# Performance work log

Measured on AMD Instinct MI355X. Metric: run time of the kernel, lower is better.

Reference implementation:

```python
import jax, jax.numpy as jnp
import numpy as np

BETA_VQ = 0.25
NUM_CODES = 1024
CODE_DIM = 256

def setup_inputs() -> dict:
    key = jax.random.key(0)
    k1, k2 = jax.random.split(key)
    z_e = jax.random.normal(k1, (64, 32, 32, CODE_DIM), dtype=jnp.float32)
    codebook = jax.random.uniform(k2, (NUM_CODES, CODE_DIM), dtype=jnp.float32,
                                  minval=-1.0 / NUM_CODES, maxval=1.0 / NUM_CODES)
    return {"z_e": z_e, "codebook": codebook}


def reference(z_e, codebook):
    B, H, W, D = z_e.shape
    z_flat = z_e.reshape(-1, D)  # [N, D], N = B*H*W
    # squared-euclidean distances via expansion: ||z||^2 + ||c||^2 - 2 z.c
    dist = (jnp.sum(z_flat ** 2, axis=1, keepdims=True)
            + jnp.sum(codebook ** 2, axis=1)
            - 2.0 * z_flat @ codebook.T)  # [N, num_codes]
    indices = jnp.argmin(dist, axis=1)  # [N]
    z_q = codebook[indices].reshape(z_e.shape)  # [B,H,W,D]
    codebook_loss = jnp.mean((jax.lax.stop_gradient(z_e) - z_q) ** 2)
    commit_loss = BETA_VQ * jnp.mean((z_e - jax.lax.stop_gradient(z_q)) ** 2)
    vq_loss = codebook_loss + commit_loss
    z_q_st = z_e + jax.lax.stop_gradient(z_q - z_e)  # straight-through
    indices = indices.reshape(B, H, W)
    return (z_q_st, vq_loss, indices)
```

## Files before the change

kernel.cpp:

```cpp
#include <hip/hip_runtime.h>
#include <hip/hip_bf16.h>


constexpr int D     = 256;
constexpr int NC    = 1024;
constexpr int NROWS = 65536;
constexpr int RPB   = 32;
constexpr int NBLK  = NROWS / RPB;
constexpr int ZS    = 264;
constexpr int QCAP  = 512;
#define MARGIN_Q 3.8e-3f

typedef float accv4  __attribute__((ext_vector_type(4)));
typedef short short8 __attribute__((ext_vector_type(8)));

__device__ __forceinline__ short f2bf(float x) {
    __hip_bfloat16 h = __float2bfloat16(x);
    return *reinterpret_cast<short*>(&h);
}
__device__ __forceinline__ unsigned packtrunc(float x, float y) {
    return (__float_as_uint(x) >> 16) | (__float_as_uint(y) & 0xffff0000u);
}

__device__ __forceinline__ float np_pairwise_sq128(const float* __restrict__ x) {
    float r[8];
    #pragma unroll
    for (int j = 0; j < 8; ++j) r[j] = __fmul_rn(x[j], x[j]);
    #pragma unroll
    for (int i = 8; i < 128; i += 8)
        #pragma unroll
        for (int j = 0; j < 8; ++j)
            r[j] = __fadd_rn(r[j], __fmul_rn(x[i + j], x[i + j]));
    float s01 = __fadd_rn(r[0], r[1]);
    float s23 = __fadd_rn(r[2], r[3]);
    float s45 = __fadd_rn(r[4], r[5]);
    float s67 = __fadd_rn(r[6], r[7]);
    return __fadd_rn(__fadd_rn(s01, s23), __fadd_rn(s45, s67));
}

__global__ void c2_kernel(const float* __restrict__ cb, float* __restrict__ c2) {
    int t = blockIdx.x * blockDim.x + threadIdx.x;
    if (t < NC) {
        const float* x = cb + (size_t)t * D;
        c2[t] = __fadd_rn(np_pairwise_sq128(x), np_pairwise_sq128(x + 128));
    }
}

__global__ void swz_kernel(const float* __restrict__ cb, short* __restrict__ swz) {
    int t = blockIdx.x * blockDim.x + threadIdx.x;
    int lane = t & 63, ts = t >> 6;
    int ks = ts & 7, tile = ts >> 3;
    int code = tile * 16 + (lane & 15);
    int kb   = ks * 32 + (lane >> 4) * 8;
    const float* src = cb + (size_t)code * D + kb;
    union { short s[8]; short8 v; } u;
    #pragma unroll
    for (int j = 0; j < 8; ++j) u.s[j] = f2bf(src[j]);
    *((short8*)swz + t) = u.v;
}

__global__ __launch_bounds__(256, 2) void vq_kernel(
    const float* __restrict__ z,
    const float* __restrict__ cb,
    const short* __restrict__ cb_swz,
    const float* __restrict__ c2g,
    float*       __restrict__ out_zq,
    float*       __restrict__ out_idx,
    double*      __restrict__ partials)
{
    __shared__ __align__(16) float z_lds[RPB][ZS];
    __shared__ float a_row[RPB];
    __shared__ __align__(16) float scratchA[RPB][4];
    __shared__ float c2_lds[NC];
    __shared__ int   rm_shared[RPB];
    __shared__ __align__(16) int queue[QCAP];
    __shared__ int   qn;

    const int tid     = threadIdx.x;
    const int lane    = tid & 63;
    const int w       = tid >> 6;
    const int rowBase = blockIdx.x * RPB;

    #pragma unroll
    for (int j = 0; j < 8; ++j) {
        int l = tid + 256 * j;
        int row = l >> 6, q = l & 63;
        float4 v = *(const float4*)(z + (size_t)(rowBase + row) * D + q * 4);
        *(float4*)&z_lds[row][q * 4] = v;
    }
    #pragma unroll
    for (int j = 0; j < 4; ++j) c2_lds[tid + 256 * j] = c2g[tid + 256 * j];
    if (tid < RPB) rm_shared[tid] = 0x7f800000;
    if (tid == 0)  qn = 0;
    __syncthreads();

    if (tid < RPB * 4) {
        int row = tid >> 2, q = tid & 3;
        int h = (q >> 1) * 128, p = (q & 1) * 4;
        const float* x = &z_lds[row][0];
        float r0 = __fmul_rn(x[h+p+0], x[h+p+0]);
        float r1 = __fmul_rn(x[h+p+1], x[h+p+1]);
        float r2 = __fmul_rn(x[h+p+2], x[h+p+2]);
        float r3 = __fmul_rn(x[h+p+3], x[h+p+3]);
        #pragma unroll
        for (int i = 8; i < 128; i += 8) {
            r0 = __fadd_rn(r0, __fmul_rn(x[h+i+p+0], x[h+i+p+0]));
            r1 = __fadd_rn(r1, __fmul_rn(x[h+i+p+1], x[h+i+p+1]));
            r2 = __fadd_rn(r2, __fmul_rn(x[h+i+p+2], x[h+i+p+2]));
            r3 = __fadd_rn(r3, __fmul_rn(x[h+i+p+3], x[h+i+p+3]));
        }
        scratchA[row][q] = __fadd_rn(__fadd_rn(r0, r1), __fadd_rn(r2, r3));
    }
    __syncthreads();
    if (tid < RPB) {
        float half0 = __fadd_rn(scratchA[tid][0], scratchA[tid][1]);
        float half1 = __fadd_rn(scratchA[tid][2], scratchA[tid][3]);
        a_row[tid]  = __fadd_rn(half0, half1);
    }
    __syncthreads();

    short8 afrag[2][8];
    #pragma unroll
    for (int rt = 0; rt < 2; ++rt)
        #pragma unroll
        for (int ks = 0; ks < 8; ++ks) {
            const float* src = z + (size_t)(rowBase + rt * 16 + (lane & 15)) * D
                                 + ks * 32 + (lane >> 4) * 8;
            float4 v0 = *(const float4*)(src);
            float4 v1 = *(const float4*)(src + 4);
            union { unsigned u[4]; short8 v; } pk;
            pk.u[0] = packtrunc(v0.x, v0.y);
            pk.u[1] = packtrunc(v0.z, v0.w);
            pk.u[2] = packtrunc(v1.x, v1.y);
            pk.u[3] = packtrunc(v1.z, v1.w);
            afrag[rt][ks] = pk.v;
        }
    float a_reg[2][4];
    #pragma unroll
    for (int rt = 0; rt < 2; ++rt)
        #pragma unroll
        for (int i = 0; i < 4; ++i)
            a_reg[rt][i] = a_row[rt * 16 + (lane >> 4) * 4 + i];

    float runmin[2][4];
    #pragma unroll
    for (int rt = 0; rt < 2; ++rt)
        #pragma unroll
        for (int i = 0; i < 4; ++i) runmin[rt][i] = 3.4e38f;

    unsigned kpk[16][2][2];
    const short8* bbase = (const short8*)cb_swz + lane;
    short8 bcur[8];
    #pragma unroll
    for (int ks = 0; ks < 8; ++ks) bcur[ks] = bbase[(size_t)w * 512 + ks * 64];

    #pragma unroll
    for (int t = 0; t < 16; ++t) {
        const int tile = w + 4 * t;
        short8 bnxt[8];
        if (t < 15) {
            #pragma unroll
            for (int ks = 0; ks < 8; ++ks)
                bnxt[ks] = bbase[(size_t)(tile + 4) * 512 + ks * 64];
        }
        accv4 acc[2];
        #pragma unroll
        for (int rt = 0; rt < 2; ++rt) acc[rt] = (accv4){0.f, 0.f, 0.f, 0.f};
        #pragma unroll
        for (int ks = 0; ks < 8; ++ks) {
            #pragma unroll
            for (int rt = 0; rt < 2; ++rt)
                acc[rt] = __builtin_amdgcn_mfma_f32_16x16x32_bf16(
                    afrag[rt][ks], bcur[ks], acc[rt], 0, 0, 0);
        }
        const float c2v = c2_lds[tile * 16 + (lane & 15)];
        #pragma unroll
        for (int rt = 0; rt < 2; ++rt) {
            float m0 = fmaf(2.0f, acc[rt][0], -c2v);
            float m1 = fmaf(2.0f, acc[rt][1], -c2v);
            float m2 = fmaf(2.0f, acc[rt][2], -c2v);
            float m3 = fmaf(2.0f, acc[rt][3], -c2v);
            kpk[t][rt][0] = packtrunc(m0, m1);
            kpk[t][rt][1] = packtrunc(m2, m3);
            runmin[rt][0] = fminf(runmin[rt][0], a_reg[rt][0] - m0);
            runmin[rt][1] = fminf(runmin[rt][1], a_reg[rt][1] - m1);
            runmin[rt][2] = fminf(runmin[rt][2], a_reg[rt][2] - m2);
            runmin[rt][3] = fminf(runmin[rt][3], a_reg[rt][3] - m3);
        }
        if (t < 15) {
            #pragma unroll
            for (int ks = 0; ks < 8; ++ks) bcur[ks] = bnxt[ks];
        }
    }

    #pragma unroll
    for (int rt = 0; rt < 2; ++rt)
        #pragma unroll
        for (int i = 0; i < 4; ++i) {
            float m = runmin[rt][i];
            m = fminf(m, __shfl_xor(m, 1));
            m = fminf(m, __shfl_xor(m, 2));
            m = fminf(m, __shfl_xor(m, 4));
            m = fminf(m, __shfl_xor(m, 8));
            if ((lane & 15) == 0) {
                int row = rt * 16 + (lane >> 4) * 4 + i;
                atomicMin(&rm_shared[row], __float_as_int(m));
            }
        }
    __syncthreads();

    float mthr[2][4];
    #pragma unroll
    for (int rt = 0; rt < 2; ++rt)
        #pragma unroll
        for (int i = 0; i < 4; ++i) {
            int row = rt * 16 + (lane >> 4) * 4 + i;
            mthr[rt][i] = a_reg[rt][i]
                        - (__int_as_float(rm_shared[row]) + MARGIN_Q);
        }
    #pragma unroll
    for (int t = 0; t < 16; ++t) {
        const int code = (w + 4 * t) * 16 + (lane & 15);
        #pragma unroll
        for (int rt = 0; rt < 2; ++rt)
            #pragma unroll
            for (int pr = 0; pr < 2; ++pr) {
                unsigned pk = kpk[t][rt][pr];
                float mlo = __uint_as_float(pk << 16);
                float mhi = __uint_as_float(pk & 0xffff0000u);
                if (mlo >= mthr[rt][2 * pr]) {
                    int row  = rt * 16 + (lane >> 4) * 4 + 2 * pr;
                    int slot = atomicAdd(&qn, 1);
                    if (slot < QCAP) queue[slot] = (row << 10) | code;
                }
                if (mhi >= mthr[rt][2 * pr + 1]) {
                    int row  = rt * 16 + (lane >> 4) * 4 + 2 * pr + 1;
                    int slot = atomicAdd(&qn, 1);
                    if (slot < QCAP) queue[slot] = (row << 10) | code;
                }
            }
    }

    unsigned long long* best64 = (unsigned long long*)&scratchA[0][0];
    if (tid < RPB) best64[tid] = ~0ull;
    __syncthreads();
    int total = qn;
    if (total <= QCAP) {
        for (int t = tid; t < total; t += 256) {
            int e = queue[t];
            int row = e >> 10, code = e & 1023;
            const float4* cp = (const float4*)(cb + (size_t)code * D);
            const float*  zr = &z_lds[row][0];
            float acc = 0.0f;
            #pragma unroll 8
            for (int d4 = 0; d4 < 64; ++d4) {
                float4 cv = cp[d4];
                acc = fmaf(zr[d4 * 4 + 0], cv.x, acc);
                acc = fmaf(zr[d4 * 4 + 1], cv.y, acc);
                acc = fmaf(zr[d4 * 4 + 2], cv.z, acc);
                acc = fmaf(zr[d4 * 4 + 3], cv.w, acc);
            }
            float key = __fsub_rn(__fadd_rn(a_row[row], c2_lds[code]), 2.0f * acc);
            unsigned long long pk =
                ((unsigned long long)__float_as_uint(key) << 32) | (unsigned)code;
            atomicMin(&best64[row], pk);
        }
    } else {
        for (int r = 0; r < RPB; ++r) {
            for (int c = tid; c < NC; c += 256) {
                const float4* cp = (const float4*)(cb + (size_t)c * D);
                const float*  zr = &z_lds[r][0];
                float acc = 0.0f;
                #pragma unroll 8
                for (int d4 = 0; d4 < 64; ++d4) {
                    float4 cv = cp[d4];
                    acc = fmaf(zr[d4 * 4 + 0], cv.x, acc);
                    acc = fmaf(zr[d4 * 4 + 1], cv.y, acc);
                    acc = fmaf(zr[d4 * 4 + 2], cv.z, acc);
                    acc = fmaf(zr[d4 * 4 + 3], cv.w, acc);
                }
                float key = __fsub_rn(__fadd_rn(a_row[r], c2_lds[c]), 2.0f * acc);
                unsigned long long pk =
                    ((unsigned long long)__float_as_uint(key) << 32) | (unsigned)c;
                atomicMin(&best64[r], pk);
            }
        }
    }
    __syncthreads();

    int* winner = rm_shared;
    if (tid < RPB) {
        unsigned long long b = best64[tid];
        int wdx = (b == ~0ull) ? 0 : (int)(b & 0xffffffffu);
        winner[tid] = wdx;
        out_idx[rowBase + tid] = (float)wdx;
    }
    __syncthreads();

    double lacc = 0.0;
    #pragma unroll
    for (int j = 0; j < 8; ++j) {
        int idx = tid + 256 * j;
        int row = idx >> 6;
        int q4  = idx & 63;
        int wd  = winner[row];
        float4 cv = *(const float4*)(cb + (size_t)wd * D + q4 * 4);
        float4 zv = *(const float4*)&z_lds[row][q4 * 4];
        float4 o;
        o.x = __fadd_rn(zv.x, __fsub_rn(cv.x, zv.x));
        o.y = __fadd_rn(zv.y, __fsub_rn(cv.y, zv.y));
        o.z = __fadd_rn(zv.z, __fsub_rn(cv.z, zv.z));
        o.w = __fadd_rn(zv.w, __fsub_rn(cv.w, zv.w));
        *(float4*)(out_zq + (size_t)(rowBase + row) * D + q4 * 4) = o;
        double d0 = (double)zv.x - (double)cv.x;
        double d1 = (double)zv.y - (double)cv.y;
        double d2 = (double)zv.z - (double)cv.z;
        double d3 = (double)zv.w - (double)cv.w;
        lacc += d0 * d0 + d1 * d1 + d2 * d2 + d3 * d3;
    }
    __syncthreads();
    double* dred = (double*)&queue[0];
    dred[tid] = lacc;
    __syncthreads();
    for (int s = 128; s > 0; s >>= 1) {
        if (tid < s) dred[tid] += dred[tid + s];
        __syncthreads();
    }
    if (tid == 0) partials[blockIdx.x] = dred[0];
}

__global__ void loss_kernel(const double* __restrict__ partials,
                            float* __restrict__ out_loss)
{
    __shared__ double sm[256];
    int tid = threadIdx.x;
    double s = 0.0;
    for (int i = tid; i < NBLK; i += 256) s += partials[i];
    sm[tid] = s;
    __syncthreads();
    for (int k = 128; k > 0; k >>= 1) {
        if (tid < k) sm[tid] += sm[tid + k];
        __syncthreads();
    }
    if (tid == 0)
        out_loss[0] = (float)(1.25 * sm[0] / (double)((size_t)NROWS * D));
}

extern "C" void kernel_launch(void* const* d_in, const int* in_sizes, int n_in,
                              void* d_out, int out_size, void* d_ws, size_t ws_size,
                              hipStream_t stream)
{
    const float* z  = (const float*)d_in[0];
    const float* cb = (const float*)d_in[1];

    float* out      = (float*)d_out;
    float* out_zq   = out;
    float* out_loss = out + (size_t)NROWS * D;
    float* out_idx  = out_loss + 1;

    char*   ws       = (char*)d_ws;
    short*  cb_swz   = (short*)ws;
    float*  c2       = (float*)(ws + 524288);
    double* partials = (double*)(ws + 528384);

    swz_kernel<<<128, 256, 0, stream>>>(cb, cb_swz);
    c2_kernel<<<4, 256, 0, stream>>>(cb, c2);
    vq_kernel<<<NBLK, 256, 0, stream>>>(z, cb, cb_swz, c2,
                                        out_zq, out_idx, partials);
    loss_kernel<<<1, 256, 0, stream>>>(partials, out_loss);
}
```

Measured before the change: 311.7 us.

## Filter candidates online after a two-tile warmup instead of storing all packed scores

```diff
diff --git a/kernel.cpp b/kernel.cpp
--- a/kernel.cpp
+++ b/kernel.cpp
@@ -8,7 +8,7 @@
 constexpr int RPB   = 32;
 constexpr int NBLK  = NROWS / RPB;
 constexpr int ZS    = 264;
-constexpr int QCAP  = 512;
+constexpr int QCAP  = 1024;
 #define MARGIN_Q 3.8e-3f
 
 typedef float accv4  __attribute__((ext_vector_type(4)));
@@ -148,21 +148,19 @@
         #pragma unroll
         for (int i = 0; i < 4; ++i) runmin[rt][i] = 3.4e38f;
 
-    unsigned kpk[16][2][2];
     const short8* bbase = (const short8*)cb_swz + lane;
     short8 bcur[8];
     #pragma unroll
     for (int ks = 0; ks < 8; ++ks) bcur[ks] = bbase[(size_t)w * 512 + ks * 64];
 
-    #pragma unroll
-    for (int t = 0; t < 16; ++t) {
+    unsigned kpk[2][2][2];
+    #pragma unroll
+    for (int t = 0; t < 2; ++t) {
         const int tile = w + 4 * t;
         short8 bnxt[8];
-        if (t < 15) {
-            #pragma unroll
-            for (int ks = 0; ks < 8; ++ks)
-                bnxt[ks] = bbase[(size_t)(tile + 4) * 512 + ks * 64];
-        }
+        #pragma unroll
+        for (int ks = 0; ks < 8; ++ks)
+            bnxt[ks] = bbase[(size_t)(tile + 4) * 512 + ks * 64];
         accv4 acc[2];
         #pragma unroll
         for (int rt = 0; rt < 2; ++rt) acc[rt] = (accv4){0.f, 0.f, 0.f, 0.f};
@@ -187,10 +185,8 @@
             runmin[rt][2] = fminf(runmin[rt][2], a_reg[rt][2] - m2);
             runmin[rt][3] = fminf(runmin[rt][3], a_reg[rt][3] - m3);
         }
-        if (t < 15) {
-            #pragma unroll
-            for (int ks = 0; ks < 8; ++ks) bcur[ks] = bnxt[ks];
-        }
+        #pragma unroll
+        for (int ks = 0; ks < 8; ++ks) bcur[ks] = bnxt[ks];
     }
 
     #pragma unroll
@@ -218,8 +214,9 @@
             mthr[rt][i] = a_reg[rt][i]
                         - (__int_as_float(rm_shared[row]) + MARGIN_Q);
         }
-    #pragma unroll
-    for (int t = 0; t < 16; ++t) {
+
+    #pragma unroll
+    for (int t = 0; t < 2; ++t) {
         const int code = (w + 4 * t) * 16 + (lane & 15);
         #pragma unroll
         for (int rt = 0; rt < 2; ++rt)
@@ -239,6 +236,69 @@
                     if (slot < QCAP) queue[slot] = (row << 10) | code;
                 }
             }
+    }
+
+    for (int t = 2; t < 16; ++t) {
+        const int tile = w + 4 * t;
+        short8 bnxt[8];
+        if (t < 15) {
+            #pragma unroll
+            for (int ks = 0; ks < 8; ++ks)
+                bnxt[ks] = bbase[(size_t)(tile + 4) * 512 + ks * 64];
+        }
+        accv4 acc[2];
+        #pragma unroll
+        for (int rt = 0; rt < 2; ++rt) acc[rt] = (accv4){0.f, 0.f, 0.f, 0.f};
+        #pragma unroll
+        for (int ks = 0; ks < 8; ++ks) {
+            #pragma unroll
+            for (int rt = 0; rt < 2; ++rt)
+                acc[rt] = __builtin_amdgcn_mfma_f32_16x16x32_bf16(
+                    afrag[rt][ks], bcur[ks], acc[rt], 0, 0, 0);
+        }
+        const float c2v  = c2_lds[tile * 16 + (lane & 15)];
+        const int   code = tile * 16 + (lane & 15);
+        #pragma unroll
+        for (int rt = 0; rt < 2; ++rt) {
+            #pragma unroll
+            for (int i = 0; i < 4; ++i) {
+                float m = fmaf(2.0f, acc[rt][i], -c2v);
+                runmin[rt][i] = fminf(runmin[rt][i], a_reg[rt][i] - m);
+                if (m >= mthr[rt][i]) {
+                    int row  = rt * 16 + (lane >> 4) * 4 + i;
+                    int slot = atomicAdd(&qn, 1);
+                    if (slot < QCAP) queue[slot] = (row << 10) | code;
+                }
+            }
+        }
+        if (t == 5 || t == 9 || t == 13) {
+            #pragma unroll
+            for (int rt = 0; rt < 2; ++rt)
+                #pragma unroll
+                for (int i = 0; i < 4; ++i) {
+                    float m = runmin[rt][i];
+                    m = fminf(m, __shfl_xor(m, 1));
+                    m = fminf(m, __shfl_xor(m, 2));
+                    m = fminf(m, __shfl_xor(m, 4));
+                    m = fminf(m, __shfl_xor(m, 8));
+                    if ((lane & 15) == 0) {
+                        int row = rt * 16 + (lane >> 4) * 4 + i;
+                        atomicMin(&rm_shared[row], __float_as_int(m));
+                    }
+                }
+            #pragma unroll
+            for (int rt = 0; rt < 2; ++rt)
+                #pragma unroll
+                for (int i = 0; i < 4; ++i) {
+                    int row = rt * 16 + (lane >> 4) * 4 + i;
+                    mthr[rt][i] = a_reg[rt][i]
+                                - (__int_as_float(rm_shared[row]) + MARGIN_Q);
+                }
+        }
+        if (t < 15) {
+            #pragma unroll
+            for (int ks = 0; ks < 8; ++ks) bcur[ks] = bnxt[ks];
+        }
     }
 
     unsigned long long* best64 = (unsigned long long*)&scratchA[0][0];
```

Measured after the change: 279.4 us. -10.4%, faster.
